# Performance work log

Hardware: AMD Instinct MI355X
Metric: run time of the kernel (lower is better)

Reference implementation:

```python
import jax, jax.numpy as jnp
import numpy as np

EMBED_DIM = 1024
N_HEADS = 16
HEAD_DIM = EMBED_DIM // N_HEADS


def setup_inputs() -> dict:
    key = jax.random.key(0)
    k_x, k_qw, k_qb, k_ow, k_ob = jax.random.split(key, 5)
    s = 1.0 / np.sqrt(EMBED_DIM)
    return {
        "x": jax.random.normal(k_x, (2, 2048, EMBED_DIM), dtype=jnp.float32),
        "qkv_w": jax.random.uniform(k_qw, (3 * EMBED_DIM, EMBED_DIM), jnp.float32, -s, s),
        "qkv_b": jax.random.uniform(k_qb, (3 * EMBED_DIM,), jnp.float32, -s, s),
        "out_w": jax.random.uniform(k_ow, (EMBED_DIM, EMBED_DIM), jnp.float32, -s, s),
        "out_b": jax.random.uniform(k_ob, (EMBED_DIM,), jnp.float32, -s, s),
    }


def reference(x, qkv_w, qkv_b, out_w, out_b):
    B, S, E = x.shape
    # fused QKV projection (torch Linear: x @ W^T + b)
    qkv = x @ qkv_w.T + qkv_b                      # [B,S,3E]
    qkv = qkv.reshape(B, S, N_HEADS, 3 * HEAD_DIM).transpose(0, 2, 1, 3)  # [B,H,S,3d]
    q, k, v = jnp.split(qkv, 3, axis=-1)           # each [B,H,S,d]
    scores = jnp.einsum("bhqd,bhkd->bhqk", q, k) / jnp.sqrt(jnp.float32(HEAD_DIM))
    weights = jax.nn.softmax(scores, axis=-1)      # [B,H,S,S]
    attn = jnp.einsum("bhqk,bhkd->bhqd", weights, v)
    attn = attn.transpose(0, 2, 1, 3).reshape(B, S, E)
    return attn @ out_w.T + out_b
```

## Files before the change

### kernel.cpp

```cpp
#include <hip/hip_runtime.h>
#include <hip/hip_bf16.h>


#define E_DIM   1024
#define NHEADS  16
#define HDIM    64
#define SEQ     2048
#define TOK     4096
#define QKV_DIM 3072

typedef __attribute__((ext_vector_type(8))) short bf16x8;
typedef __attribute__((ext_vector_type(4))) float f32x4;
typedef __attribute__((ext_vector_type(4))) int   i32x4;
typedef __attribute__((ext_vector_type(2))) int   i32x2;
typedef __attribute__((ext_vector_type(4))) unsigned short u16x4;
typedef __attribute__((ext_vector_type(2))) __bf16 bf16x2_t;

__device__ __forceinline__ unsigned short f2bf(float x) {
    union { float f; unsigned u; } a; a.f = x;
    unsigned r = a.u + 0x7FFF + ((a.u >> 16) & 1);
    return (unsigned short)(r >> 16);
}

__device__ __forceinline__ unsigned pack2bf(float a, float b) {
#if __has_builtin(__builtin_amdgcn_cvt_pk_bf16_f32)
    union { bf16x2_t v; unsigned u; } u;
    u.v = __builtin_amdgcn_cvt_pk_bf16_f32(a, b);
    return u.u;
#else
    union { float f; unsigned u; } ua, ub; ua.f = a; ub.f = b;
    unsigned ra = ua.u + 0x7FFF + ((ua.u >> 16) & 1);
    unsigned rb = ub.u + 0x7FFF + ((ub.u >> 16) & 1);
    return (ra >> 16) | (rb & 0xFFFF0000u);
#endif
}

__device__ __forceinline__ void load_lds16(const void* g, void* l) {
    __builtin_amdgcn_global_load_lds(
        (const __attribute__((address_space(1))) void*)g,
        (__attribute__((address_space(3))) void*)l, 16, 0, 0);
}

__device__ __forceinline__ bf16x8 lds_read8(const unsigned short* p) {
    union { i32x4 i; bf16x8 b; } u;
    u.i = *(const i32x4*)p;
    return u.b;
}

__device__ __forceinline__ f32x4 mfma16(bf16x8 a, bf16x8 b, f32x4 c) {
    return __builtin_amdgcn_mfma_f32_16x16x32_bf16(a, b, c, 0, 0, 0);
}

__global__ void cast_bf16_kernel(const float* __restrict__ in,
                                 unsigned short* __restrict__ out, int n4) {
    int i = blockIdx.x * blockDim.x + threadIdx.x;
    if (i >= n4) return;
    f32x4 v = ((const f32x4*)in)[i];
    union { i32x2 i2; unsigned u[2]; } o;
    o.u[0] = pack2bf(v.x, v.y);
    o.u[1] = pack2bf(v.z, v.w);
    ((i32x2*)out)[i] = o.i2;
}

template<bool BF16_OUT>
__global__ __launch_bounds__(256, 2)
void gemm_bt_kernel(const unsigned short* __restrict__ A,
                    const unsigned short* __restrict__ B,
                    const float* __restrict__ bias,
                    void* __restrict__ C, int M, int N, int K) {
    __shared__ __align__(16) unsigned short As[128 * 64];
    __shared__ __align__(16) unsigned short Bs[128 * 64];

    const int tid  = threadIdx.x;
    const int wave = tid >> 6, lane = tid & 63;
    const int quad = lane >> 4, l16 = lane & 15;
    const int row0 = blockIdx.y * 128, col0 = blockIdx.x * 128;
    const int wr = (wave >> 1) * 64, wc = (wave & 1) * 64;

    f32x4 acc[4][4];
#pragma unroll
    for (int i = 0; i < 4; ++i)
#pragma unroll
        for (int j = 0; j < 4; ++j) acc[i][j] = (f32x4){0.f, 0.f, 0.f, 0.f};

    const int nkt = K >> 6;
    for (int kt = 0; kt < nkt; ++kt) {
        const int k0 = kt << 6;
#pragma unroll
        for (int i = 0; i < 4; ++i) {
            int p = i * 256 + tid;
            int r = p >> 3;
            int kc = (p & 7) ^ (r & 7);
            load_lds16(A + (size_t)(row0 + r) * K + k0 + kc * 8, &As[p * 8]);
        }
#pragma unroll
        for (int i = 0; i < 4; ++i) {
            int p = i * 256 + tid;
            int r = p >> 3;
            int kc = (p & 7) ^ (r & 7);
            load_lds16(B + (size_t)(col0 + r) * K + k0 + kc * 8, &Bs[p * 8]);
        }
        __syncthreads();

#pragma unroll
        for (int ks = 0; ks < 2; ++ks) {
            bf16x8 af[4], bfr[4];
#pragma unroll
            for (int rb = 0; rb < 4; ++rb) {
                int r_l  = wr + rb * 16 + l16;
                int phys = (ks * 4 + quad) ^ (l16 & 7);
                af[rb] = lds_read8(&As[r_l * 64 + phys * 8]);
            }
#pragma unroll
            for (int cb = 0; cb < 4; ++cb) {
                int r_l  = wc + cb * 16 + l16;
                int phys = (ks * 4 + quad) ^ (l16 & 7);
                bfr[cb] = lds_read8(&Bs[r_l * 64 + phys * 8]);
            }
#pragma unroll
            for (int rb = 0; rb < 4; ++rb)
#pragma unroll
                for (int cb = 0; cb < 4; ++cb)
                    acc[rb][cb] = mfma16(af[rb], bfr[cb], acc[rb][cb]);
        }
        __syncthreads();
    }

#pragma unroll
    for (int rb = 0; rb < 4; ++rb)
#pragma unroll
        for (int cb = 0; cb < 4; ++cb) {
            int col = col0 + wc + cb * 16 + l16;
            float bv = bias[col];
#pragma unroll
            for (int reg = 0; reg < 4; ++reg) {
                int row = row0 + wr + rb * 16 + quad * 4 + reg;
                float v = acc[rb][cb][reg] + bv;
                if (BF16_OUT)
                    ((unsigned short*)C)[(size_t)row * N + col] = f2bf(v);
                else
                    ((float*)C)[(size_t)row * N + col] = v;
            }
        }
}

__global__ __launch_bounds__(256, 4)
void gemm_bt64_kernel(const unsigned short* __restrict__ A,
                      const unsigned short* __restrict__ B,
                      const float* __restrict__ bias,
                      float* __restrict__ C, int M, int N, int K) {
    __shared__ __align__(16) unsigned short As[64 * 64];
    __shared__ __align__(16) unsigned short Bs[64 * 64];

    const int tid  = threadIdx.x;
    const int wave = tid >> 6, lane = tid & 63;
    const int quad = lane >> 4, l16 = lane & 15;
    const int row0 = blockIdx.y * 64, col0 = blockIdx.x * 64;
    const int wr = (wave >> 1) * 32, wc = (wave & 1) * 32;

    f32x4 acc[2][2];
#pragma unroll
    for (int i = 0; i < 2; ++i)
#pragma unroll
        for (int j = 0; j < 2; ++j) acc[i][j] = (f32x4){0.f, 0.f, 0.f, 0.f};

    const int nkt = K >> 6;
    for (int kt = 0; kt < nkt; ++kt) {
        const int k0 = kt << 6;
#pragma unroll
        for (int i = 0; i < 2; ++i) {
            int p = i * 256 + tid;
            int r = p >> 3;
            int kc = (p & 7) ^ (r & 7);
            load_lds16(A + (size_t)(row0 + r) * K + k0 + kc * 8, &As[p * 8]);
        }
#pragma unroll
        for (int i = 0; i < 2; ++i) {
            int p = i * 256 + tid;
            int r = p >> 3;
            int kc = (p & 7) ^ (r & 7);
            load_lds16(B + (size_t)(col0 + r) * K + k0 + kc * 8, &Bs[p * 8]);
        }
        __syncthreads();

#pragma unroll
        for (int ks = 0; ks < 2; ++ks) {
            bf16x8 af[2], bfr[2];
#pragma unroll
            for (int rb = 0; rb < 2; ++rb) {
                int r_l  = wr + rb * 16 + l16;
                int phys = (ks * 4 + quad) ^ (l16 & 7);
                af[rb] = lds_read8(&As[r_l * 64 + phys * 8]);
            }
#pragma unroll
            for (int cb = 0; cb < 2; ++cb) {
                int r_l  = wc + cb * 16 + l16;
                int phys = (ks * 4 + quad) ^ (l16 & 7);
                bfr[cb] = lds_read8(&Bs[r_l * 64 + phys * 8]);
            }
#pragma unroll
            for (int rb = 0; rb < 2; ++rb)
#pragma unroll
                for (int cb = 0; cb < 2; ++cb)
                    acc[rb][cb] = mfma16(af[rb], bfr[cb], acc[rb][cb]);
        }
        __syncthreads();
    }

#pragma unroll
    for (int rb = 0; rb < 2; ++rb)
#pragma unroll
        for (int cb = 0; cb < 2; ++cb) {
            int col = col0 + wc + cb * 16 + l16;
            float bv = bias[col];
#pragma unroll
            for (int reg = 0; reg < 4; ++reg) {
                int row = row0 + wr + rb * 16 + quad * 4 + reg;
                C[(size_t)row * N + col] = acc[rb][cb][reg] + bv;
            }
        }
}

__global__ __launch_bounds__(256)
void vtrans_kernel(const unsigned short* __restrict__ qkv,
                   unsigned short* __restrict__ vT) {
    __shared__ __align__(16) unsigned short T[64 * 72];
    const int tid = threadIdx.x;
    const int bh = blockIdx.y, b = bh >> 4, h = bh & 15;
    const int s0 = blockIdx.x * 64;

    const int tok = tid & 63;
    const int ic0 = tid >> 6;
#pragma unroll
    for (int it = 0; it < 2; ++it) {
        int chunk = it * 4 + ic0;
        const unsigned short* p =
            qkv + ((size_t)(b * SEQ + s0 + tok)) * QKV_DIM + h * 192 + 128 + chunk * 8;
        union { i32x4 v; unsigned short s[8]; } va;
        va.v = *(const i32x4*)p;
#pragma unroll
        for (int j = 0; j < 8; ++j)
            T[(chunk * 8 + j) * 72 + tok] = va.s[j];
    }
    __syncthreads();

#pragma unroll
    for (int it = 0; it < 2; ++it) {
        int p = it * 256 + tid;
        int r = p >> 3, c = (p & 7) * 8;
        i32x4 v = *(const i32x4*)&T[r * 72 + c];
        *(i32x4*)&vT[((size_t)bh * 64 + r) * SEQ + s0 + c] = v;
    }
}

__global__ __launch_bounds__(512, 4)
void attn_kernel(const unsigned short* __restrict__ qkv,
                 const unsigned short* __restrict__ vT,
                 unsigned short* __restrict__ attn) {
    __shared__ __align__(16) unsigned short Ks[128 * 64];
    __shared__ __align__(16) unsigned short Vs[64 * 128];
    __shared__ __align__(16) unsigned short Ps[8][16 * 72];

    const int tid  = threadIdx.x;
    const int wave = tid >> 6, lane = tid & 63;
    const int quad = lane >> 4, l16 = lane & 15;
    const int bh = blockIdx.y;
    const int b = bh >> 4, h = bh & 15;
    const int q0 = blockIdx.x * 128;
    const size_t rowbase = (size_t)b * SEQ;
    const int qtok = q0 + wave * 16 + l16;

    bf16x8 qf[2];
#pragma unroll
    for (int ks = 0; ks < 2; ++ks) {
        const unsigned short* p =
            qkv + (rowbase + qtok) * QKV_DIM + h * 192 + ks * 32 + quad * 8;
        union { i32x4 i; bf16x8 b; } u;
        u.i = *(const i32x4*)p;
        qf[ks] = u.b;
    }

    f32x4 o[4];
#pragma unroll
    for (int ib = 0; ib < 4; ++ib) o[ib] = (f32x4){0.f, 0.f, 0.f, 0.f};
    float l_s = 0.f;

    const float cexp = 0.125f * 1.44269504088896340736f;

    for (int kt = 0; kt < SEQ / 128; ++kt) {
        const int kb = kt * 128;
#pragma unroll
        for (int i = 0; i < 2; ++i) {
            int p = i * 512 + tid;
            int r = p >> 3;
            int kc = (p & 7) ^ (r & 7);
            load_lds16(qkv + (rowbase + kb + r) * QKV_DIM + h * 192 + 64 + kc * 8,
                       &Ks[p * 8]);
        }
#pragma unroll
        for (int i = 0; i < 2; ++i) {
            int p = i * 512 + tid;
            int r = p >> 4;
            int c = (p & 15) ^ (r & 15);
            load_lds16(vT + ((size_t)bh * 64 + r) * SEQ + kb + c * 8, &Vs[p * 8]);
        }
        __syncthreads();

        f32x4 s[8];
#pragma unroll
        for (int cb = 0; cb < 8; ++cb) s[cb] = (f32x4){0.f, 0.f, 0.f, 0.f};
#pragma unroll
        for (int ks = 0; ks < 2; ++ks)
#pragma unroll
            for (int cb = 0; cb < 8; ++cb) {
                int row  = cb * 16 + l16;
                int phys = (ks * 4 + quad) ^ (l16 & 7);
                bf16x8 kf = lds_read8(&Ks[row * 64 + phys * 8]);
                s[cb] = mfma16(kf, qf[ks], s[cb]);
            }

        float rs = 0.f;
#pragma unroll
        for (int cb = 0; cb < 8; ++cb)
#pragma unroll
            for (int r = 0; r < 4; ++r) {
                float pv = exp2f(s[cb][r] * cexp);
                s[cb][r] = pv;
                rs += pv;
            }
        rs += __shfl_xor(rs, 16);
        rs += __shfl_xor(rs, 32);
        l_s += rs;

#pragma unroll
        for (int half = 0; half < 2; ++half) {
#pragma unroll
            for (int c4 = 0; c4 < 4; ++c4) {
                int cb = half * 4 + c4;
                i32x2 pk;
                pk.x = (int)pack2bf(s[cb][0], s[cb][1]);
                pk.y = (int)pack2bf(s[cb][2], s[cb][3]);
                *(i32x2*)&Ps[wave][l16 * 72 + c4 * 16 + quad * 4] = pk;
            }
            __asm__ volatile("s_waitcnt lgkmcnt(0)" ::: "memory");
#pragma unroll
            for (int kc2 = 0; kc2 < 2; ++kc2) {
                bf16x8 pf = lds_read8(&Ps[wave][l16 * 72 + kc2 * 32 + quad * 8]);
#pragma unroll
                for (int ib = 0; ib < 4; ++ib) {
                    int row  = ib * 16 + l16;
                    int kcl  = half * 8 + kc2 * 4 + quad;
                    int phys = kcl ^ l16;
                    bf16x8 vf = lds_read8(&Vs[row * 128 + phys * 8]);
                    o[ib] = mfma16(pf, vf, o[ib]);
                }
            }
        }
        __syncthreads();
    }

    float il[4];
#pragma unroll
    for (int r = 0; r < 4; ++r) il[r] = 1.0f / __shfl(l_s, quad * 4 + r);
#pragma unroll
    for (int ib = 0; ib < 4; ++ib)
#pragma unroll
        for (int r = 0; r < 4; ++r) {
            int t = q0 + wave * 16 + quad * 4 + r;
            attn[(rowbase + t) * E_DIM + h * 64 + ib * 16 + l16] =
                f2bf(o[ib][r] * il[r]);
        }
}

extern "C" void kernel_launch(void* const* d_in, const int* in_sizes, int n_in,
                              void* d_out, int out_size, void* d_ws, size_t ws_size,
                              hipStream_t stream) {
    const float* x     = (const float*)d_in[0];
    const float* qkv_w = (const float*)d_in[1];
    const float* qkv_b = (const float*)d_in[2];
    const float* out_w = (const float*)d_in[3];
    const float* out_b = (const float*)d_in[4];

    char* ws = (char*)d_ws;
    unsigned short* xb   = (unsigned short*)(ws);
    unsigned short* wqkv = (unsigned short*)(ws + 8388608);
    unsigned short* wout = (unsigned short*)(ws + 14680064);
    unsigned short* qkv  = (unsigned short*)(ws + 16777216);
    unsigned short* attn = (unsigned short*)(ws + 41943040);
    unsigned short* vT   = xb;

    cast_bf16_kernel<<<4096, 256, 0, stream>>>(x, xb, 1048576);
    cast_bf16_kernel<<<3072, 256, 0, stream>>>(qkv_w, wqkv, 786432);
    cast_bf16_kernel<<<1024, 256, 0, stream>>>(out_w, wout, 262144);

    gemm_bt_kernel<true><<<dim3(24, 32), 256, 0, stream>>>(
        xb, wqkv, qkv_b, (void*)qkv, TOK, QKV_DIM, E_DIM);

    vtrans_kernel<<<dim3(32, 32), 256, 0, stream>>>(qkv, vT);

    attn_kernel<<<dim3(16, 32), 512, 0, stream>>>(qkv, vT, attn);

    gemm_bt64_kernel<<<dim3(16, 64), 256, 0, stream>>>(
        attn, wout, out_b, (float*)d_out, TOK, E_DIM, E_DIM);
}
```

Measured before the change: 217.3 us.

## Merge casts, fold softmax scale into QKV GEMM, retile attention and output GEMM

Merges the three bf16 cast launches into one kernel and folds the 1/sqrt(d)*log2e softmax scale into the Q columns of the QKV GEMM epilogue, so the attention kernel no longer multiplies each score. Attention changes from 512-thread blocks over 128 queries to 256-thread blocks over 64 queries, with LDS offsets precomputed in registers and a swizzled P buffer replacing the padded one. The output projection moves from 64x64 to 128x64 tiles. The extra attention blocks reload K/V tiles more often, and the precomputed offsets raise register pressure.

```diff
diff --git a/kernel.cpp b/kernel.cpp
--- a/kernel.cpp
+++ b/kernel.cpp
@@ -8,12 +8,12 @@
 #define SEQ     2048
 #define TOK     4096
 #define QKV_DIM 3072
+#define QSCALE_F 0.18033688011112042f
 
 typedef __attribute__((ext_vector_type(8))) short bf16x8;
 typedef __attribute__((ext_vector_type(4))) float f32x4;
 typedef __attribute__((ext_vector_type(4))) int   i32x4;
 typedef __attribute__((ext_vector_type(2))) int   i32x2;
-typedef __attribute__((ext_vector_type(4))) unsigned short u16x4;
 typedef __attribute__((ext_vector_type(2))) __bf16 bf16x2_t;
 
 __device__ __forceinline__ unsigned short f2bf(float x) {
@@ -51,18 +51,22 @@
     return __builtin_amdgcn_mfma_f32_16x16x32_bf16(a, b, c, 0, 0, 0);
 }
 
-__global__ void cast_bf16_kernel(const float* __restrict__ in,
-                                 unsigned short* __restrict__ out, int n4) {
+__global__ void cast3_kernel(const float* __restrict__ a, unsigned short* __restrict__ oa, int na4,
+                             const float* __restrict__ b, unsigned short* __restrict__ ob, int nb4,
+                             const float* __restrict__ c, unsigned short* __restrict__ oc) {
     int i = blockIdx.x * blockDim.x + threadIdx.x;
-    if (i >= n4) return;
-    f32x4 v = ((const f32x4*)in)[i];
+    const float* src; unsigned short* dst; int j;
+    if (i < na4)            { src = a; dst = oa; j = i; }
+    else if (i < na4 + nb4) { src = b; dst = ob; j = i - na4; }
+    else                    { src = c; dst = oc; j = i - na4 - nb4; }
+    f32x4 v = ((const f32x4*)src)[j];
     union { i32x2 i2; unsigned u[2]; } o;
     o.u[0] = pack2bf(v.x, v.y);
     o.u[1] = pack2bf(v.z, v.w);
-    ((i32x2*)out)[i] = o.i2;
-}
-
-template<bool BF16_OUT>
+    ((i32x2*)dst)[j] = o.i2;
+}
+
+template<bool BF16_OUT, bool QSCALE>
 __global__ __launch_bounds__(256, 2)
 void gemm_bt_kernel(const unsigned short* __restrict__ A,
                     const unsigned short* __restrict__ B,
@@ -132,10 +136,11 @@
         for (int cb = 0; cb < 4; ++cb) {
             int col = col0 + wc + cb * 16 + l16;
             float bv = bias[col];
+            float sc = (QSCALE && (col % 192) < 64) ? QSCALE_F : 1.0f;
 #pragma unroll
             for (int reg = 0; reg < 4; ++reg) {
                 int row = row0 + wr + rb * 16 + quad * 4 + reg;
-                float v = acc[rb][cb][reg] + bv;
+                float v = (acc[rb][cb][reg] + bv) * sc;
                 if (BF16_OUT)
                     ((unsigned short*)C)[(size_t)row * N + col] = f2bf(v);
                 else
@@ -144,31 +149,31 @@
         }
 }
 
-__global__ __launch_bounds__(256, 4)
-void gemm_bt64_kernel(const unsigned short* __restrict__ A,
-                      const unsigned short* __restrict__ B,
-                      const float* __restrict__ bias,
-                      float* __restrict__ C, int M, int N, int K) {
-    __shared__ __align__(16) unsigned short As[64 * 64];
+__global__ __launch_bounds__(256, 2)
+void gemm2_kernel(const unsigned short* __restrict__ A,
+                  const unsigned short* __restrict__ B,
+                  const float* __restrict__ bias,
+                  float* __restrict__ C, int M, int N, int K) {
+    __shared__ __align__(16) unsigned short As[128 * 64];
     __shared__ __align__(16) unsigned short Bs[64 * 64];
 
     const int tid  = threadIdx.x;
     const int wave = tid >> 6, lane = tid & 63;
     const int quad = lane >> 4, l16 = lane & 15;
-    const int row0 = blockIdx.y * 64, col0 = blockIdx.x * 64;
-    const int wr = (wave >> 1) * 32, wc = (wave & 1) * 32;
-
-    f32x4 acc[2][2];
+    const int row0 = blockIdx.y * 128, col0 = blockIdx.x * 64;
+    const int wr = wave * 32;
+
+    f32x4 acc[2][4];
 #pragma unroll
     for (int i = 0; i < 2; ++i)
 #pragma unroll
-        for (int j = 0; j < 2; ++j) acc[i][j] = (f32x4){0.f, 0.f, 0.f, 0.f};
+        for (int j = 0; j < 4; ++j) acc[i][j] = (f32x4){0.f, 0.f, 0.f, 0.f};
 
     const int nkt = K >> 6;
     for (int kt = 0; kt < nkt; ++kt) {
         const int k0 = kt << 6;
 #pragma unroll
-        for (int i = 0; i < 2; ++i) {
+        for (int i = 0; i < 4; ++i) {
             int p = i * 256 + tid;
             int r = p >> 3;
             int kc = (p & 7) ^ (r & 7);
@@ -185,7 +190,7 @@
 
 #pragma unroll
         for (int ks = 0; ks < 2; ++ks) {
-            bf16x8 af[2], bfr[2];
+            bf16x8 af[2], bfr[4];
 #pragma unroll
             for (int rb = 0; rb < 2; ++rb) {
                 int r_l  = wr + rb * 16 + l16;
@@ -193,15 +198,15 @@
                 af[rb] = lds_read8(&As[r_l * 64 + phys * 8]);
             }
 #pragma unroll
-            for (int cb = 0; cb < 2; ++cb) {
-                int r_l  = wc + cb * 16 + l16;
+            for (int cb = 0; cb < 4; ++cb) {
+                int r_l  = cb * 16 + l16;
                 int phys = (ks * 4 + quad) ^ (l16 & 7);
                 bfr[cb] = lds_read8(&Bs[r_l * 64 + phys * 8]);
             }
 #pragma unroll
             for (int rb = 0; rb < 2; ++rb)
 #pragma unroll
-                for (int cb = 0; cb < 2; ++cb)
+                for (int cb = 0; cb < 4; ++cb)
                     acc[rb][cb] = mfma16(af[rb], bfr[cb], acc[rb][cb]);
         }
         __syncthreads();
@@ -210,8 +215,8 @@
 #pragma unroll
     for (int rb = 0; rb < 2; ++rb)
 #pragma unroll
-        for (int cb = 0; cb < 2; ++cb) {
-            int col = col0 + wc + cb * 16 + l16;
+        for (int cb = 0; cb < 4; ++cb) {
+            int col = col0 + cb * 16 + l16;
             float bv = bias[col];
 #pragma unroll
             for (int reg = 0; reg < 4; ++reg) {
@@ -253,22 +258,52 @@
     }
 }
 
-__global__ __launch_bounds__(512, 4)
+__global__ __launch_bounds__(256, 4)
 void attn_kernel(const unsigned short* __restrict__ qkv,
                  const unsigned short* __restrict__ vT,
                  unsigned short* __restrict__ attn) {
     __shared__ __align__(16) unsigned short Ks[128 * 64];
     __shared__ __align__(16) unsigned short Vs[64 * 128];
-    __shared__ __align__(16) unsigned short Ps[8][16 * 72];
+    __shared__ __align__(16) unsigned short Ps[4][16 * 64];
 
     const int tid  = threadIdx.x;
     const int wave = tid >> 6, lane = tid & 63;
     const int quad = lane >> 4, l16 = lane & 15;
     const int bh = blockIdx.y;
     const int b = bh >> 4, h = bh & 15;
-    const int q0 = blockIdx.x * 128;
+    const int q0 = blockIdx.x * 64;
     const size_t rowbase = (size_t)b * SEQ;
     const int qtok = q0 + wave * 16 + l16;
+
+    int koff[2][8];
+#pragma unroll
+    for (int ks = 0; ks < 2; ++ks)
+#pragma unroll
+        for (int cb = 0; cb < 8; ++cb)
+            koff[ks][cb] = (cb * 16 + l16) * 64 + (((ks * 4 + quad) ^ (l16 & 7)) * 8);
+    int voff[4][4];
+#pragma unroll
+    for (int hk = 0; hk < 4; ++hk)
+#pragma unroll
+        for (int ib = 0; ib < 4; ++ib)
+            voff[hk][ib] = (ib * 16 + l16) * 128 + (((hk * 4 + quad) ^ l16) * 8);
+    int pwoff[4];
+#pragma unroll
+    for (int c4 = 0; c4 < 4; ++c4)
+        pwoff[c4] = l16 * 64 + (((c4 * 2 + (quad >> 1)) ^ (l16 & 7)) * 8) + (quad & 1) * 4;
+    int proff[2];
+#pragma unroll
+    for (int kc2 = 0; kc2 < 2; ++kc2)
+        proff[kc2] = l16 * 64 + (((kc2 * 4 + quad) ^ (l16 & 7)) * 8);
+    int skoff[4], svoff[4];
+#pragma unroll
+    for (int i = 0; i < 4; ++i) {
+        int p = i * 256 + tid;
+        int rk = p >> 3;
+        skoff[i] = rk * QKV_DIM + ((p & 7) ^ (rk & 7)) * 8;
+        int rv = p >> 4;
+        svoff[i] = rv * SEQ + ((p & 15) ^ (rv & 15)) * 8;
+    }
 
     bf16x8 qf[2];
 #pragma unroll
@@ -285,25 +320,16 @@
     for (int ib = 0; ib < 4; ++ib) o[ib] = (f32x4){0.f, 0.f, 0.f, 0.f};
     float l_s = 0.f;
 
-    const float cexp = 0.125f * 1.44269504088896340736f;
-
     for (int kt = 0; kt < SEQ / 128; ++kt) {
         const int kb = kt * 128;
-#pragma unroll
-        for (int i = 0; i < 2; ++i) {
-            int p = i * 512 + tid;
-            int r = p >> 3;
-            int kc = (p & 7) ^ (r & 7);
-            load_lds16(qkv + (rowbase + kb + r) * QKV_DIM + h * 192 + 64 + kc * 8,
-                       &Ks[p * 8]);
-        }
-#pragma unroll
-        for (int i = 0; i < 2; ++i) {
-            int p = i * 512 + tid;
-            int r = p >> 4;
-            int c = (p & 15) ^ (r & 15);
-            load_lds16(vT + ((size_t)bh * 64 + r) * SEQ + kb + c * 8, &Vs[p * 8]);
-        }
+        const unsigned short* kbase = qkv + (rowbase + kb) * QKV_DIM + h * 192 + 64;
+        const unsigned short* vbase = vT + (size_t)bh * 64 * SEQ + kb;
+#pragma unroll
+        for (int i = 0; i < 4; ++i)
+            load_lds16(kbase + skoff[i], &Ks[(i * 256 + tid) * 8]);
+#pragma unroll
+        for (int i = 0; i < 4; ++i)
+            load_lds16(vbase + svoff[i], &Vs[(i * 256 + tid) * 8]);
         __syncthreads();
 
         f32x4 s[8];
@@ -313,9 +339,7 @@
         for (int ks = 0; ks < 2; ++ks)
 #pragma unroll
             for (int cb = 0; cb < 8; ++cb) {
-                int row  = cb * 16 + l16;
-                int phys = (ks * 4 + quad) ^ (l16 & 7);
-                bf16x8 kf = lds_read8(&Ks[row * 64 + phys * 8]);
+                bf16x8 kf = lds_read8(&Ks[koff[ks][cb]]);
                 s[cb] = mfma16(kf, qf[ks], s[cb]);
             }
 
@@ -324,7 +348,7 @@
         for (int cb = 0; cb < 8; ++cb)
 #pragma unroll
             for (int r = 0; r < 4; ++r) {
-                float pv = exp2f(s[cb][r] * cexp);
+                float pv = exp2f(s[cb][r]);
                 s[cb][r] = pv;
                 rs += pv;
             }
@@ -340,18 +364,15 @@
                 i32x2 pk;
                 pk.x = (int)pack2bf(s[cb][0], s[cb][1]);
                 pk.y = (int)pack2bf(s[cb][2], s[cb][3]);
-                *(i32x2*)&Ps[wave][l16 * 72 + c4 * 16 + quad * 4] = pk;
+                *(i32x2*)&Ps[wave][pwoff[c4]] = pk;
             }
             __asm__ volatile("s_waitcnt lgkmcnt(0)" ::: "memory");
 #pragma unroll
             for (int kc2 = 0; kc2 < 2; ++kc2) {
-                bf16x8 pf = lds_read8(&Ps[wave][l16 * 72 + kc2 * 32 + quad * 8]);
+                bf16x8 pf = lds_read8(&Ps[wave][proff[kc2]]);
 #pragma unroll
                 for (int ib = 0; ib < 4; ++ib) {
-                    int row  = ib * 16 + l16;
-                    int kcl  = half * 8 + kc2 * 4 + quad;
-                    int phys = kcl ^ l16;
-                    bf16x8 vf = lds_read8(&Vs[row * 128 + phys * 8]);
+                    bf16x8 vf = lds_read8(&Vs[voff[half * 2 + kc2][ib]]);
                     o[ib] = mfma16(pf, vf, o[ib]);
                 }
             }
@@ -389,17 +410,17 @@
     unsigned short* attn = (unsigned short*)(ws + 41943040);
     unsigned short* vT   = xb;
 
-    cast_bf16_kernel<<<4096, 256, 0, stream>>>(x, xb, 1048576);
-    cast_bf16_kernel<<<3072, 256, 0, stream>>>(qkv_w, wqkv, 786432);
-    cast_bf16_kernel<<<1024, 256, 0, stream>>>(out_w, wout, 262144);
-
-    gemm_bt_kernel<true><<<dim3(24, 32), 256, 0, stream>>>(
+    cast3_kernel<<<8192, 256, 0, stream>>>(x, xb, 1048576,
+                                           qkv_w, wqkv, 786432,
+                                           out_w, wout);
+
+    gemm_bt_kernel<true, true><<<dim3(24, 32), 256, 0, stream>>>(
         xb, wqkv, qkv_b, (void*)qkv, TOK, QKV_DIM, E_DIM);
 
     vtrans_kernel<<<dim3(32, 32), 256, 0, stream>>>(qkv, vT);
 
-    attn_kernel<<<dim3(16, 32), 512, 0, stream>>>(qkv, vT, attn);
-
-    gemm_bt64_kernel<<<dim3(16, 64), 256, 0, stream>>>(
+    attn_kernel<<<dim3(32, 32), 256, 0, stream>>>(qkv, vT, attn);
+
+    gemm2_kernel<<<dim3(16, 32), 256, 0, stream>>>(
         attn, wout, out_b, (float*)d_out, TOK, E_DIM, E_DIM);
 }
```

After: 216.3 us. About the same (-0.4%).
